# Performance work log

Hardware: AMD Instinct MI355X
Metric: run time of the kernel (lower is better)

Reference implementation:

```python
import jax, jax.numpy as jnp
import numpy as np

D, H, KVH, HD = 2048, 16, 8, 128
D1, D2 = 32, 64  # get_decompose_dim(2048)
BITS = 8


def fake_quant(x, bits=BITS):
    # per-row (last-axis) symmetric fake quant with straight-through estimator
    qmax = float(2 ** (bits - 1) - 1)
    s = jnp.maximum(jnp.max(jnp.abs(x), axis=-1, keepdims=True) / qmax, 1e-8)
    q = jnp.clip(jnp.round(x / s), -qmax, qmax) * s
    return x + jax.lax.stop_gradient(q - x)


def rotate_half(x):
    h = x.shape[-1] // 2
    return jnp.concatenate([-x[..., h:], x[..., :h]], axis=-1)


def setup_inputs() -> dict:
    key = jax.random.key(0)
    ks = jax.random.split(key, 10)
    B, S = 1, 2048
    hidden_states = jax.random.normal(ks[0], (B, S, D), jnp.float32)
    # rotary embeddings
    inv_freq = 1.0 / (10000.0 ** (jnp.arange(0, HD, 2, dtype=jnp.float32) / HD))
    t = jnp.arange(S, dtype=jnp.float32)
    freqs = t[:, None] * inv_freq[None, :]
    emb = jnp.concatenate([freqs, freqs], axis=-1)
    cos, sin = jnp.cos(emb)[None], jnp.sin(emb)[None]  # [1,S,HD]
    # projection weights
    Wq = jax.random.normal(ks[1], (H * HD, D), jnp.float32) * 0.02
    Wk = jax.random.normal(ks[2], (KVH * HD, D), jnp.float32) * 0.02
    Wv = jax.random.normal(ks[3], (KVH * HD, D), jnp.float32) * 0.02
    Wo = jax.random.normal(ks[4], (D, H * HD), jnp.float32) * 0.02
    # learned invertible transforms (near-identity for conditioning)
    L = jnp.eye(D1) + 0.02 * jax.random.normal(ks[5], (D1, D1), jnp.float32)
    R = jnp.eye(D2) + 0.02 * jax.random.normal(ks[6], (D2, D2), jnp.float32)
    diag = 1.0 + 0.1 * jax.random.uniform(ks[7], (D,), jnp.float32)
    Tk = jnp.eye(HD) + 0.02 * jax.random.normal(ks[8], (HD, HD), jnp.float32)
    Tv = jnp.eye(HD) + 0.02 * jax.random.normal(ks[9], (HD, HD), jnp.float32)
    return dict(hidden_states=hidden_states, cos=cos, sin=sin, Wq=Wq, Wk=Wk,
                Wv=Wv, Wo=Wo, L=L, R=R, diag=diag, Tk=Tk, Tv=Tv)


def reference(hidden_states, cos, sin, Wq, Wk, Wv, Wo, L, R, diag, Tk, Tv):
    B, S, _ = hidden_states.shape
    groups = H // KVH
    scale = HD ** -0.5
    # ---- ln_trans: x' = (x * diag) @ kron(L, R) ----
    P = diag[:, None] * jnp.kron(L, R)               # [D, D]
    Pinv = jnp.kron(jnp.linalg.inv(L), jnp.linalg.inv(R)) * (1.0 / diag)[None, :]
    x = hidden_states @ P
    x_q = fake_quant(x)                               # per-token activation quant
    # ---- QKV with transform fused into weights (qa_trans), then weight quant ----
    q = x_q @ fake_quant(Wq @ Pinv.T).T               # [B,S,H*HD]
    k = x_q @ fake_quant(Wk @ Pinv.T).T               # [B,S,KVH*HD]
    Wv_eff = jnp.einsum('hd,khD->kdD', Tv, (Wv @ Pinv.T).reshape(KVH, HD, D))
    v = x_q @ fake_quant(Wv_eff.reshape(KVH * HD, D)).T  # v already in Tv space
    # ---- heads + RoPE ----
    q = q.reshape(B, S, H, HD).transpose(0, 2, 1, 3)
    k = k.reshape(B, S, KVH, HD).transpose(0, 2, 1, 3)
    v = v.reshape(B, S, KVH, HD).transpose(0, 2, 1, 3)
    c, s_ = cos[:, None], sin[:, None]                # [1,1,S,HD]
    q = q * c + rotate_half(q) * s_
    k = k * c + rotate_half(k) * s_
    # ---- kcache trans + quant: q @ inv(Tk)^T, k @ Tk (dot product preserved) ----
    q = q @ jnp.linalg.inv(Tk).T
    k = fake_quant(k @ Tk)
    v = fake_quant(v)
    # ---- eager causal attention with GQA ----
    k = jnp.repeat(k, groups, axis=1)
    v = jnp.repeat(v, groups, axis=1)
    scores = jnp.einsum('bhqd,bhkd->bhqk', q, k) * scale
    mask = jnp.tril(jnp.ones((S, S), bool))
    scores = jnp.where(mask, scores, jnp.finfo(scores.dtype).min)
    w = jax.nn.softmax(scores, axis=-1)
    o = jnp.einsum('bhqk,bhkd->bhqd', w, v)
    o = o.transpose(0, 2, 1, 3).reshape(B, S, H * HD)
    # ---- undo vcache trans per head, then quantized o_proj ----
    o = (o.reshape(B, S, H, HD) @ jnp.linalg.inv(Tv)).reshape(B, S, H * HD)
    out = fake_quant(o) @ fake_quant(Wo).T
    return out
```

## Files before the change

### kernel.cpp

```cpp
#include <hip/hip_runtime.h>
#include <math.h>

typedef unsigned short u16;
typedef __attribute__((ext_vector_type(8))) short bf16x8;
typedef __attribute__((ext_vector_type(4))) float f32x4;

__device__ __forceinline__ u16 f2bf(float x) {
    union { float f; unsigned int u; } c; c.f = x;
    unsigned int r = c.u + 0x7fffu + ((c.u >> 16) & 1u);
    return (u16)(r >> 16);
}
__device__ __forceinline__ float bf2f(u16 h) {
    union { unsigned int u; float f; } c; c.u = ((unsigned int)h) << 16;
    return c.f;
}
__device__ __forceinline__ bf16x8 ld16(const u16* p) {
    bf16x8 r;
    ((uint2*)&r)[0] = *(const uint2*)p;
    ((uint2*)&r)[1] = *(const uint2*)(p + 4);
    return r;
}
__device__ __forceinline__ void st8(u16* dst, uint4 r) {
    *(uint2*)dst = make_uint2(r.x, r.y);
    *(uint2*)(dst + 4) = make_uint2(r.z, r.w);
}
__device__ __forceinline__ void cvt8(const float4& v0, const float4& v1,
                                     uint4& hi, uint4& lo) {
    float vv[8] = {v0.x, v0.y, v0.z, v0.w, v1.x, v1.y, v1.z, v1.w};
    u16 h[8], l[8];
#pragma unroll
    for (int e = 0; e < 8; ++e) {
        h[e] = f2bf(vv[e]);
        l[e] = f2bf(vv[e] - bf2f(h[e]));
    }
    hi.x = h[0] | ((unsigned)h[1] << 16); hi.y = h[2] | ((unsigned)h[3] << 16);
    hi.z = h[4] | ((unsigned)h[5] << 16); hi.w = h[6] | ((unsigned)h[7] << 16);
    lo.x = l[0] | ((unsigned)l[1] << 16); lo.y = l[2] | ((unsigned)l[3] << 16);
    lo.z = l[4] | ((unsigned)l[5] << 16); lo.w = l[6] | ((unsigned)l[7] << 16);
}

__global__ __launch_bounds__(1024) void p0_kernel(
    const float* __restrict__ A0, float* __restrict__ I0,
    const float* __restrict__ A1, float* __restrict__ I1,
    const float* __restrict__ A2, float* __restrict__ I2,
    const float* __restrict__ A3, float* __restrict__ I3,
    const float* __restrict__ X, const float* __restrict__ dg,
    const float* __restrict__ Lk, const float* __restrict__ Rk,
    u16* __restrict__ Yq, float* __restrict__ Ysc) {
    const int tid = threadIdx.x;
    if (blockIdx.x < 4) {
        __shared__ float rowbuf[2][128];
        const float* A; float* out; int N;
        switch (blockIdx.x) {
            case 0:  A = A0; out = I0; N = 32;  break;
            case 1:  A = A1; out = I1; N = 64;  break;
            case 2:  A = A2; out = I2; N = 128; break;
            default: A = A3; out = I3; N = 128; break;
        }
        const int i = tid >> 3, g = tid & 7, c0 = g * 16;
        const int rl = (i & 7) << 3;
        float r[16];
#pragma unroll
        for (int e = 0; e < 16; ++e) {
            int j = c0 + e;
            r[e] = (i < N && j < N) ? A[i * N + j] : ((i == j) ? 1.0f : 0.0f);
        }
        if (i == 0) {
            float ip = 1.0f / __shfl(r[0], rl, 64);
#pragma unroll
            for (int e = 0; e < 16; ++e)
                rowbuf[0][c0 + e] = (c0 + e == 0) ? ip : r[e] * ip;
        }
        __syncthreads();
        const int ng = N >> 4;
        for (int k16 = 0; k16 < ng; ++k16) {
#pragma unroll
            for (int e = 0; e < 16; ++e) {
                const int k = (k16 << 4) + e;
                const int pb = k & 1;
                float ci = __shfl(r[e], rl + k16, 64);
                float4 rb0 = *(const float4*)&rowbuf[pb][c0];
                float4 rb1 = *(const float4*)&rowbuf[pb][c0 + 4];
                float4 rb2 = *(const float4*)&rowbuf[pb][c0 + 8];
                float4 rb3 = *(const float4*)&rowbuf[pb][c0 + 12];
                float rb[16] = {rb0.x, rb0.y, rb0.z, rb0.w, rb1.x, rb1.y, rb1.z, rb1.w,
                                rb2.x, rb2.y, rb2.z, rb2.w, rb3.x, rb3.y, rb3.z, rb3.w};
                if (i == k) {
#pragma unroll
                    for (int e2 = 0; e2 < 16; ++e2) r[e2] = rb[e2];
                } else {
#pragma unroll
                    for (int e2 = 0; e2 < 16; ++e2) {
                        float v = (c0 + e2 == k) ? 0.0f : r[e2];
                        r[e2] = fmaf(-ci, rb[e2], v);
                    }
                }
                if (k + 1 < N && i == k + 1) {
                    const int en = (e + 1) & 15;
                    const int gn = (e == 15) ? k16 + 1 : k16;
                    float ip = 1.0f / __shfl(r[en], rl + gn, 64);
#pragma unroll
                    for (int e2 = 0; e2 < 16; ++e2)
                        rowbuf[pb ^ 1][c0 + e2] = (c0 + e2 == k + 1) ? ip : r[e2] * ip;
                }
                __syncthreads();
            }
        }
        if (i < N)
#pragma unroll
            for (int e = 0; e < 16; ++e) {
                int j = c0 + e;
                if (j < N) out[i * N + j] = r[e];
            }
    } else {
        __shared__ float Al[32 * 33];
        __shared__ float Bl[64 * 65];
        __shared__ float Tl[4][32 * 65];
        __shared__ float red[1024];
        {
            int c = tid >> 5, a = tid & 31;
            Al[c * 33 + a] = Lk[c * 32 + a];
        }
        for (int idx = tid; idx < 4096; idx += 1024) {
            int d = idx >> 6, b = idx & 63;
            Bl[d * 65 + b] = Rk[d * 64 + b];
        }
        __syncthreads();

        const int g = tid >> 8, t = tid & 255;
        const int row = (blockIdx.x - 4) * 4 + g;
        const int c = t >> 3, b0 = (t & 7) * 8;

        const float* xp = X + (size_t)row * 2048 + c * 64;
        const float* dgp = dg + c * 64;
        float tacc[8];
#pragma unroll
        for (int jj = 0; jj < 8; ++jj) tacc[jj] = 0.0f;
        for (int d0 = 0; d0 < 64; d0 += 4) {
            float4 xv4 = *(const float4*)(xp + d0);
            float4 dg4 = *(const float4*)(dgp + d0);
            float xs4[4] = {xv4.x * dg4.x, xv4.y * dg4.y, xv4.z * dg4.z, xv4.w * dg4.w};
#pragma unroll
            for (int e = 0; e < 4; ++e) {
                float xv = xs4[e];
#pragma unroll
                for (int jj = 0; jj < 8; ++jj)
                    tacc[jj] = fmaf(xv, Bl[(d0 + e) * 65 + b0 + jj], tacc[jj]);
            }
        }
#pragma unroll
        for (int jj = 0; jj < 8; ++jj) Tl[g][c * 65 + b0 + jj] = tacc[jj];
        __syncthreads();

        const int a = t >> 3;
        float y[8];
#pragma unroll
        for (int jj = 0; jj < 8; ++jj) y[jj] = 0.0f;
        for (int c2 = 0; c2 < 32; ++c2) {
            float av = Al[c2 * 33 + a];
#pragma unroll
            for (int jj = 0; jj < 8; ++jj)
                y[jj] = fmaf(av, Tl[g][c2 * 65 + b0 + jj], y[jj]);
        }

        float am = 0.0f;
#pragma unroll
        for (int jj = 0; jj < 8; ++jj) am = fmaxf(am, fabsf(y[jj]));
        red[tid] = am;
        __syncthreads();
        for (int s = 128; s > 0; s >>= 1) {
            if (t < s) red[tid] = fmaxf(red[tid], red[tid + s]);
            __syncthreads();
        }
        float scale = fmaxf(red[g << 8] / 127.0f, 1e-8f);
        if (t == 0) Ysc[row] = scale;
        u16 qq[8];
#pragma unroll
        for (int e = 0; e < 8; ++e) {
            float v = rintf(y[e] / scale);
            v = fminf(fmaxf(v, -127.0f), 127.0f);
            qq[e] = f2bf(v);
        }
        uint4 pk;
        pk.x = qq[0] | ((unsigned)qq[1] << 16); pk.y = qq[2] | ((unsigned)qq[3] << 16);
        pk.z = qq[4] | ((unsigned)qq[5] << 16); pk.w = qq[6] | ((unsigned)qq[7] << 16);
        *(uint4*)(Yq + (size_t)row * 2048 + t * 8) = pk;
    }
}

template <int TA, int TB, int OUTQ, int DIV>
__global__ __launch_bounds__(256) void kron_kernel(
    const float* __restrict__ X, const float* __restrict__ scIn,
    const float* __restrict__ A, const float* __restrict__ B,
    u16* __restrict__ Yq, float* __restrict__ Ysc, float* __restrict__ Yf) {
    __shared__ float Al[32 * 33];
    __shared__ float Bl[64 * 65];
    __shared__ float Xl[32 * 65];
    __shared__ float Tl[32 * 65];
    __shared__ float red[256];
    const int tid = threadIdx.x;
    for (int idx = tid; idx < 1024; idx += 256) {
        int c = idx >> 5, a = idx & 31;
        Al[c * 33 + a] = TA ? A[a * 32 + c] : A[c * 32 + a];
    }
    for (int idx = tid; idx < 4096; idx += 256) {
        int d = idx >> 6, b = idx & 63;
        Bl[d * 65 + b] = TB ? B[b * 64 + d] : B[d * 64 + b];
    }
    const int row = blockIdx.x;
    const float* xp = X + (size_t)row * 2048;
    for (int j = tid; j < 2048; j += 256) {
        float sc = DIV ? (1.0f / scIn[j]) : scIn[j];
        Xl[(j >> 6) * 65 + (j & 63)] = xp[j] * sc;
    }
    __syncthreads();

    const int c = tid >> 3, b0 = (tid & 7) * 8;
    float t[8];
#pragma unroll
    for (int jj = 0; jj < 8; ++jj) t[jj] = 0.0f;
    for (int d = 0; d < 64; ++d) {
        float xv = Xl[c * 65 + d];
#pragma unroll
        for (int jj = 0; jj < 8; ++jj)
            t[jj] = fmaf(xv, Bl[d * 65 + b0 + jj], t[jj]);
    }
#pragma unroll
    for (int jj = 0; jj < 8; ++jj) Tl[c * 65 + b0 + jj] = t[jj];
    __syncthreads();

    const int a = tid >> 3;
    float y[8];
#pragma unroll
    for (int jj = 0; jj < 8; ++jj) y[jj] = 0.0f;
    for (int c2 = 0; c2 < 32; ++c2) {
        float av = Al[c2 * 33 + a];
#pragma unroll
        for (int jj = 0; jj < 8; ++jj)
            y[jj] = fmaf(av, Tl[c2 * 65 + b0 + jj], y[jj]);
    }

    if (OUTQ) {
        float am = 0.0f;
#pragma unroll
        for (int jj = 0; jj < 8; ++jj) am = fmaxf(am, fabsf(y[jj]));
        red[tid] = am;
        __syncthreads();
        for (int s = 128; s > 0; s >>= 1) {
            if (tid < s) red[tid] = fmaxf(red[tid], red[tid + s]);
            __syncthreads();
        }
        float scale = fmaxf(red[0] / 127.0f, 1e-8f);
        if (tid == 0) Ysc[row] = scale;
        u16 qq[8];
#pragma unroll
        for (int e = 0; e < 8; ++e) {
            float v = rintf(y[e] / scale);
            v = fminf(fmaxf(v, -127.0f), 127.0f);
            qq[e] = f2bf(v);
        }
        uint4 pk;
        pk.x = qq[0] | ((unsigned)qq[1] << 16); pk.y = qq[2] | ((unsigned)qq[3] << 16);
        pk.z = qq[4] | ((unsigned)qq[5] << 16); pk.w = qq[6] | ((unsigned)qq[7] << 16);
        *(uint4*)(Yq + (size_t)row * 2048 + tid * 8) = pk;
    } else {
        float* yp = Yf + (size_t)row * 2048 + tid * 8;
        *(float4*)yp = make_float4(y[0], y[1], y[2], y[3]);
        *(float4*)(yp + 4) = make_float4(y[4], y[5], y[6], y[7]);
    }
}

__global__ void split_s_kernel(const float* __restrict__ in, int ld, int cols,
                               u16* __restrict__ hi, u16* __restrict__ lo) {
    int idx = (blockIdx.x * 256 + threadIdx.x) * 4;
    int r = idx / cols, c = idx % cols;
    float4 v = *(const float4*)(in + (size_t)r * ld + c);
    ushort4 h, l;
    h.x = f2bf(v.x); l.x = f2bf(v.x - bf2f(h.x));
    h.y = f2bf(v.y); l.y = f2bf(v.y - bf2f(h.y));
    h.z = f2bf(v.z); l.z = f2bf(v.z - bf2f(h.z));
    h.w = f2bf(v.w); l.w = f2bf(v.w - bf2f(h.w));
    *(ushort4*)(hi + idx) = h;
    *(ushort4*)(lo + idx) = l;
}

__global__ void split_t_kernel(const float* __restrict__ in, u16* __restrict__ hi,
                               u16* __restrict__ lo, int rows, int cols) {
    __shared__ float t[32][33];
    int bx = blockIdx.x, by = blockIdx.y;
    int lx = threadIdx.x & 31, ly = threadIdx.x >> 5;
    for (int r = ly; r < 32; r += 8)
        t[r][lx] = in[(size_t)(by * 32 + r) * cols + bx * 32 + lx];
    __syncthreads();
    for (int r = ly; r < 32; r += 8) {
        float v = t[lx][r];
        size_t o = (size_t)(bx * 32 + r) * rows + by * 32 + lx;
        u16 h = f2bf(v);
        hi[o] = h;
        lo[o] = f2bf(v - bf2f(h));
    }
}

__global__ void split_t3_kernel(const float* __restrict__ i0, u16* __restrict__ h0,
                                u16* __restrict__ l0,
                                const float* __restrict__ i1, u16* __restrict__ h1,
                                u16* __restrict__ l1,
                                const float* __restrict__ i2, u16* __restrict__ h2,
                                u16* __restrict__ l2) {
    __shared__ float t[32][33];
    const float* in; u16* hi; u16* lo;
    switch (blockIdx.z) {
        case 0:  in = i0; hi = h0; lo = l0; break;
        case 1:  in = i1; hi = h1; lo = l1; break;
        default: in = i2; hi = h2; lo = l2; break;
    }
    int bx = blockIdx.x, by = blockIdx.y;
    int lx = threadIdx.x & 31, ly = threadIdx.x >> 5;
    for (int r = ly; r < 32; r += 8)
        t[r][lx] = in[(size_t)(by * 32 + r) * 128 + bx * 32 + lx];
    __syncthreads();
    for (int r = ly; r < 32; r += 8) {
        float v = t[lx][r];
        size_t o = (size_t)(bx * 32 + r) * 128 + by * 32 + lx;
        u16 h = f2bf(v);
        hi[o] = h;
        lo[o] = f2bf(v - bf2f(h));
    }
}

__global__ __launch_bounds__(256) void gemm_kernel(
    const u16* __restrict__ Ah, const u16* __restrict__ Al, int lda, long aZ, int aDiv,
    const u16* __restrict__ Bh, const u16* __restrict__ Bl, int ldb, long bZ, int bDiv,
    float* __restrict__ C, int ldc, long cZ, int cDiv, int K, float alpha) {
    const int m0 = blockIdx.y * 128, n0 = blockIdx.x * 128;
    const int z = blockIdx.z;
    {
        long ao = (long)(z >> aDiv) * aZ;
        long bo = (long)(z >> bDiv) * bZ;
        Ah += ao; Al += ao; Bh += bo; Bl += bo;
    }
    __shared__ u16 Ash[2][2][128][36];
    __shared__ u16 Bsh[2][2][128][36];

    const int tid = threadIdx.x, lane = tid & 63, wave = tid >> 6;
    const int wr = wave >> 1, wc = wave & 1;
    const int fr = lane & 15, fg8 = (lane >> 4) * 8;
    const int srow = tid >> 2, cc8 = (tid & 3) * 8;

    f32x4 acc[4][4];
#pragma unroll
    for (int m = 0; m < 4; ++m)
#pragma unroll
        for (int n = 0; n < 4; ++n) acc[m][n] = (f32x4)0.0f;

    uint4 rah0, rah1, ral0, ral1, rbh0, rbh1, rbl0, rbl1;
    const size_t aoff0 = (size_t)(m0 + srow) * lda + cc8;
    const size_t aoff1 = aoff0 + (size_t)64 * lda;
    const size_t boff0 = (size_t)(n0 + srow) * ldb + cc8;
    const size_t boff1 = boff0 + (size_t)64 * ldb;

#define G_LOAD(k0) { \
    rah0 = *(const uint4*)(Ah + aoff0 + (k0)); rah1 = *(const uint4*)(Ah + aoff1 + (k0)); \
// ... 22 lines not shown
#pragma unroll
        for (int m = 0; m < 4; ++m) {
            bf16x8 ah = ld16(&Ash[cur][0][wr * 64 + m * 16 + fr][fg8]);
            bf16x8 al = ld16(&Ash[cur][1][wr * 64 + m * 16 + fr][fg8]);
#pragma unroll
            for (int n = 0; n < 4; ++n) {
                acc[m][n] = __builtin_amdgcn_mfma_f32_16x16x32_bf16(ah, bh[n], acc[m][n], 0, 0, 0);
                acc[m][n] = __builtin_amdgcn_mfma_f32_16x16x32_bf16(ah, bl[n], acc[m][n], 0, 0, 0);
                acc[m][n] = __builtin_amdgcn_mfma_f32_16x16x32_bf16(al, bh[n], acc[m][n], 0, 0, 0);
            }
        }
        if (ik + 1 < nk) G_STORE(cur ^ 1);
        __syncthreads();
        cur ^= 1;
    }
    const long co = (long)(z >> cDiv) * cZ;
#pragma unroll
    for (int m = 0; m < 4; ++m) {
        int row_b = m0 + wr * 64 + m * 16 + (fg8 >> 1);
#pragma unroll
        for (int n = 0; n < 4; ++n) {
            int col = n0 + wc * 64 + n * 16 + fr;
#pragma unroll
            for (int j = 0; j < 4; ++j)
                C[co + (long)(row_b + j) * ldc + col] = alpha * acc[m][n][j];
        }
    }
#undef G_LOAD
#undef G_STORE
}

__global__ __launch_bounds__(256) void gemm_qk_kernel(
    const float* __restrict__ QKVf,
    const u16* __restrict__ iTk_h, const u16* __restrict__ iTk_l,
    const u16* __restrict__ TkT_h, const u16* __restrict__ TkT_l,
    float* __restrict__ q2f, float* __restrict__ k2f) {
    const int m0 = blockIdx.y * 128;
    const int z = blockIdx.z;
    const bool isQ = (z < 16);
    const float* A = QKVf + (isQ ? z * 128 : 2048 + (z - 16) * 128);
    const u16* Bh = isQ ? iTk_h : TkT_h;
    const u16* Bl = isQ ? iTk_l : TkT_l;
    float* C = isQ ? (q2f + z * 128) : (k2f + (z - 16) * 128);
    const int ldc = isQ ? 2048 : 1024;
    const int lda = 4096, ldb = 128, K = 128;

    __shared__ u16 Ash[2][2][128][36];
    __shared__ u16 Bsh[2][2][128][36];
    const int tid = threadIdx.x, lane = tid & 63, wave = tid >> 6;
    const int wr = wave >> 1, wc = wave & 1;
    const int fr = lane & 15, fg8 = (lane >> 4) * 8;
    const int srow = tid >> 2, cc8 = (tid & 3) * 8;

    f32x4 acc[4][4];
#pragma unroll
    for (int m = 0; m < 4; ++m)
#pragma unroll
        for (int n = 0; n < 4; ++n) acc[m][n] = (f32x4)0.0f;

    float4 a00, a01, a10, a11;
    uint4 rbh0, rbh1, rbl0, rbl1;
    const size_t aoff0 = (size_t)(m0 + srow) * lda + cc8;
    const size_t aoff1 = aoff0 + (size_t)64 * lda;
    const size_t boff0 = (size_t)srow * ldb + cc8;
    const size_t boff1 = boff0 + (size_t)64 * ldb;

#define GQ_LOAD(k0) { \
    a00 = *(const float4*)(A + aoff0 + (k0)); a01 = *(const float4*)(A + aoff0 + (k0) + 4); \
    a10 = *(const float4*)(A + aoff1 + (k0)); a11 = *(const float4*)(A + aoff1 + (k0) + 4); \
    rbh0 = *(const uint4*)(Bh + boff0 + (k0)); rbh1 = *(const uint4*)(Bh + boff1 + (k0)); \
    rbl0 = *(const uint4*)(Bl + boff0 + (k0)); rbl1 = *(const uint4*)(Bl + boff1 + (k0)); }
#define GQ_STORE(b) { \
    uint4 h0_, l0_, h1_, l1_; \
    cvt8(a00, a01, h0_, l0_); cvt8(a10, a11, h1_, l1_); \
    st8(&Ash[b][0][srow][cc8], h0_); st8(&Ash[b][0][srow + 64][cc8], h1_); \
    st8(&Ash[b][1][srow][cc8], l0_); st8(&Ash[b][1][srow + 64][cc8], l1_); \
    st8(&Bsh[b][0][srow][cc8], rbh0); st8(&Bsh[b][0][srow + 64][cc8], rbh1); \
    st8(&Bsh[b][1][srow][cc8], rbl0); st8(&Bsh[b][1][srow + 64][cc8], rbl1); }

    const int nk = K >> 5;
    GQ_LOAD(0);
    GQ_STORE(0);
    __syncthreads();
    int cur = 0;
    for (int ik = 0; ik < nk; ++ik) {
        if (ik + 1 < nk) GQ_LOAD((ik + 1) << 5);
        bf16x8 bh[4], bl[4];
#pragma unroll
        for (int n = 0; n < 4; ++n) {
            bh[n] = ld16(&Bsh[cur][0][wc * 64 + n * 16 + fr][fg8]);
            bl[n] = ld16(&Bsh[cur][1][wc * 64 + n * 16 + fr][fg8]);
        }
#pragma unroll
        for (int m = 0; m < 4; ++m) {
            bf16x8 ah = ld16(&Ash[cur][0][wr * 64 + m * 16 + fr][fg8]);
            bf16x8 al = ld16(&Ash[cur][1][wr * 64 + m * 16 + fr][fg8]);
#pragma unroll
            for (int n = 0; n < 4; ++n) {
                acc[m][n] = __builtin_amdgcn_mfma_f32_16x16x32_bf16(ah, bh[n], acc[m][n], 0, 0, 0);
                acc[m][n] = __builtin_amdgcn_mfma_f32_16x16x32_bf16(ah, bl[n], acc[m][n], 0, 0, 0);
                acc[m][n] = __builtin_amdgcn_mfma_f32_16x16x32_bf16(al, bh[n], acc[m][n], 0, 0, 0);
            }
        }
        if (ik + 1 < nk) GQ_STORE(cur ^ 1);
        __syncthreads();
        cur ^= 1;
    }
#pragma unroll
    for (int m = 0; m < 4; ++m) {
        int row_b = m0 + wr * 64 + m * 16 + (fg8 >> 1);
#pragma unroll
        for (int n = 0; n < 4; ++n) {
            int col = wc * 64 + n * 16 + fr;
#pragma unroll
            for (int j = 0; j < 4; ++j)
                C[(long)(row_b + j) * ldc + col] = acc[m][n][j];
        }
    }
#undef GQ_LOAD
#undef GQ_STORE
}

__global__ __launch_bounds__(256) void gemm_o2_kernel(
    const float* __restrict__ o01, const float* __restrict__ ml,
    const u16* __restrict__ Bh, const u16* __restrict__ Bl,
    float* __restrict__ C) {
    const int m0 = blockIdx.y * 128;
    const int z = blockIdx.z;
    const int ldb = 128, K = 128, ldc = 2048;
    __shared__ u16 Ash[2][2][128][36];
    __shared__ u16 Bsh[2][2][128][36];
    const int tid = threadIdx.x, lane = tid & 63, wave = tid >> 6;
    const int wr = wave >> 1, wc = wave & 1;
    const int fr = lane & 15, fg8 = (lane >> 4) * 8;
    const int srow = tid >> 2, cc8 = (tid & 3) * 8;

    f32x4 acc[4][4];
#pragma unroll
    for (int m = 0; m < 4; ++m)
#pragma unroll
        for (int n = 0; n < 4; ++n) acc[m][n] = (f32x4)0.0f;

    const int rs0 = z * 2048 + m0 + srow;
    const int rs1 = rs0 + 64;
    float w0a, w1a, w0b, w1b;
    {
        float ma0 = ml[rs0], la0 = ml[32768 + rs0];
        float ma1 = ml[65536 + rs0], la1 = ml[98304 + rs0];
        float mm = fmaxf(ma0, ma1);
        float e0 = exp2f(ma0 - mm), e1 = exp2f(ma1 - mm);
        float linv = 1.0f / (la0 * e0 + la1 * e1);
        w0a = e0 * linv; w1a = e1 * linv;
        float mb0 = ml[rs1], lb0 = ml[32768 + rs1];
// ... 227 lines not shown
        vr[q] = *(const float4*)(p + q * 4);
        m = fmaxf(m, fmaxf(fmaxf(fabsf(vr[q].x), fabsf(vr[q].y)),
                           fmaxf(fabsf(vr[q].z), fabsf(vr[q].w))));
    }
    m = fmaxf(m, __shfl_xor(m, 1));
    m = fmaxf(m, __shfl_xor(m, 2));
    float scale = fmaxf(m / 127.0f, 1e-8f);
    if ((t & 3) == 0) vs[s * 8 + g] = scale;
#pragma unroll
    for (int q = 0; q < 8; ++q) {
        float vv[4] = {vr[q].x, vr[q].y, vr[q].z, vr[q].w};
#pragma unroll
        for (int e = 0; e < 4; ++e) {
            float qv = rintf(vv[e] / scale);
            qv = fminf(fmaxf(qv, -127.0f), 127.0f);
            tile[dc + q * 4 + e][sl] = f2bf(qv);
        }
    }
    __syncthreads();
    const int d = t >> 1, sc0 = (t & 1) * 32;
    u16* dst = vTi + (size_t)(g * 128 + d) * 2048 + st * 64 + sc0;
#pragma unroll
    for (int q = 0; q < 4; ++q) {
        u16 tmp[8];
#pragma unroll
        for (int e = 0; e < 8; ++e) tmp[e] = tile[d][sc0 + q * 8 + e];
        uint4 v;
        v.x = tmp[0] | ((unsigned)tmp[1] << 16); v.y = tmp[2] | ((unsigned)tmp[3] << 16);
        v.z = tmp[4] | ((unsigned)tmp[5] << 16); v.w = tmp[6] | ((unsigned)tmp[7] << 16);
        *(uint4*)(dst + q * 8) = v;
    }
}

__global__ void rope_kernel(float* __restrict__ x, int ld, int cb,
                            const float* __restrict__ c, const float* __restrict__ s,
                            int nh) {
    int idx = blockIdx.x * 256 + threadIdx.x;
    int d = idx & 63;
    int t = idx >> 6;
    int h = t % nh;
    int sq = t / nh;
    size_t base = (size_t)sq * ld + cb + h * 128;
    float a = x[base + d], b = x[base + d + 64];
    float c1 = c[sq * 128 + d], s1 = s[sq * 128 + d];
    float c2 = c[sq * 128 + d + 64], s2 = s[sq * 128 + d + 64];
    x[base + d] = a * c1 - b * s1;
    x[base + d + 64] = b * c2 + a * s2;
}

__global__ void add2_kernel(const float* __restrict__ a, const float* __restrict__ b,
                            float* __restrict__ o) {
    int i = (blockIdx.x * 256 + threadIdx.x) * 4;
    float4 x = *(const float4*)(a + i);
    float4 y = *(const float4*)(b + i);
    x.x += y.x; x.y += y.y; x.z += y.z; x.w += y.w;
    *(float4*)(o + i) = x;
}

__global__ __launch_bounds__(256, 2) void flash_kernel(
    const float* __restrict__ q2f,
    const u16* __restrict__ k2i, const float* __restrict__ ksc,
    const u16* __restrict__ vTi, const float* __restrict__ vsc,
    float* __restrict__ obuf, float* __restrict__ mlbuf) {
    const int h = blockIdx.x, part = blockIdx.y, qt = 31 - blockIdx.z, g = h >> 1;
    __shared__ u16 Ksh[2][64 * 128];
    __shared__ u16 Vsh[2][128 * 64];
    __shared__ u16 Psh[4][16 * 64];
    __shared__ float Kss[2][64];
    __shared__ float Vss[2][64];

    const int tid = threadIdx.x, lane = tid & 63, w = tid >> 6;
    const int lc = lane & 15, lg = lane >> 4;
    const float scale = 0.08838834764831845f;
    const float LOG2E = 1.4426950408889634f;
    const float THR = 10.0f;

    bf16x8 qh[4], ql[4];
    {
        int s = qt * 64 + w * 16 + lc;
        const float* qp = q2f + (size_t)s * 2048 + h * 128 + lg * 8;
#pragma unroll
        for (int kk = 0; kk < 4; ++kk) {
// ... 180 lines not shown
    const float* diag   = (const float*)d_in[9];
    const float* Tkp    = (const float*)d_in[10];
    const float* Tvp    = (const float*)d_in[11];
    float* out = (float*)d_out;

    const size_t MiB = 1ull << 20;
    char* W = (char*)d_ws;
    auto F = [&](size_t mb) { return (float*)(W + mb * MiB); };
    auto U = [&](size_t mb) { return (u16*)(W + mb * MiB); };
    const long HP2 = 2097152;

    float* dsc   = (float*)d_out;
    float* invL  = dsc;
    float* invR  = dsc + 1024;
    float* invTk = dsc + 5120;
    float* invTv = dsc + 21504;
    u16* sm = (u16*)(dsc + 37888);
    u16* invTk_sh = sm;              u16* invTk_sl = sm + 16384;
    u16* TkT_sh   = sm + 2 * 16384;  u16* TkT_sl   = sm + 3 * 16384;
    u16* invTvT_sh= sm + 4 * 16384;  u16* invTvT_sl= sm + 5 * 16384;
    u16* TvT_sh   = sm + 6 * 16384;  u16* TvT_sl   = sm + 7 * 16384;

    float* xs    = F(88);
    float* wqkvs = xs + 2048;
    float* wqs   = wqkvs;
    float* wks   = wqkvs + 2048;
    float* wvs   = wqkvs + 3072;
    float* k2s   = wqkvs + 4096;
    float* vs    = k2s + 16384;
    float* o2s   = vs + 16384;
    float* wos   = o2s + 2048;

    u16* Xi = U(0);
    p0_kernel<<<516, 1024, 0, stream>>>(Lp, invL, Rp, invR, Tkp, invTk, Tvp, invTv,
                                        hidden, diag, Lp, Rp, Xi, xs);
    split_s_kernel<<<16, 256, 0, stream>>>(invTk, 128, 128, invTk_sh, invTk_sl);
    split_t3_kernel<<<dim3(4, 4, 3), 256, 0, stream>>>(
        Tkp, TkT_sh, TkT_sl, invTv, invTvT_sh, invTvT_sl, Tvp, TvT_sh, TvT_sl);

    u16* WQKVi = U(8);
    u16* WVi   = U(20);
    float* WvP = F(24);
    kron_kernel<1, 1, 1, 1><<<2048, 256, 0, stream>>>(Wq, diag, invL, invR, WQKVi, wqs, 0);
    kron_kernel<1, 1, 1, 1><<<1024, 256, 0, stream>>>(Wk, diag, invL, invR, U(16), wks, 0);
    kron_kernel<1, 1, 0, 1><<<1024, 256, 0, stream>>>(Wv, diag, invL, invR, 0, 0, WvP);

    u16* WVPt_s = U(32);
    split_t_kernel<<<dim3(64, 32), 256, 0, stream>>>(WvP, WVPt_s, WVPt_s + HP2, 1024, 2048);
    float* WVf = F(72);
    gemm_kernel<<<dim3(16, 1, 8), 256, 0, stream>>>(
        TvT_sh, TvT_sl, 128, 0, 0, WVPt_s, WVPt_s + HP2, 1024, 128, 0,
        WVf, 2048, (long)128 * 2048, 0, 128, 1.0f);
    rowquant_int_kernel<<<1024, 256, 0, stream>>>(WVf, WVi, wvs, 2048);

    float* QKVf = F(40);
    gemm_int_kernel<<<dim3(32, 16), 256, 0, stream>>>(Xi, 2048, xs, WQKVi, 2048, wqkvs,
                                                      QKVf, 4096, 0, 0, 0, 2048);

    rope_kernel<<<8192, 256, 0, stream>>>(QKVf, 4096, 0, cosp, sinp, 16);
    rope_kernel<<<4096, 256, 0, stream>>>(QKVf, 4096, 2048, cosp, sinp, 8);

    float* q2f = F(72);
    float* k2f = F(32);
    gemm_qk_kernel<<<dim3(1, 16, 24), 256, 0, stream>>>(
        QKVf, invTk_sh, invTk_sl, TkT_sh, TkT_sl, q2f, k2f);
    u16* k2i = U(8);
    rowquant_w_kernel<<<4096, 256, 0, stream>>>(k2f, k2i, k2s);

    u16* vTi = U(16);
    quantT_v_kernel<<<dim3(32, 8), 256, 0, stream>>>(QKVf, vTi, vs);

    float* o01 = F(40);
    float* ml  = F(32);
    flash_kernel<<<dim3(16, 2, 32), 256, 0, stream>>>(q2f, k2i, k2s, vTi, vs, o01, ml);

    float* o2f = F(16);
    gemm_o2_kernel<<<dim3(1, 16, 16), 256, 0, stream>>>(
        o01, ml, invTvT_sh, invTvT_sl, o2f);
    u16* o2i = U(32);
    u16* Woi = U(40);
    rowquant2_kernel<<<4096, 256, 0, stream>>>(o2f, o2i, o2s, Wo, Woi, wos);
    float* C0 = F(48);
    gemm_int_kernel<<<dim3(16, 16, 2), 256, 0, stream>>>(o2i, 2048, o2s, Woi, 2048, wos,
                                                         C0, 2048, 1024, 1024, 4194304, 1024);
    add2_kernel<<<4096, 256, 0, stream>>>(C0, C0 + 4194304, out);

    (void)in_sizes; (void)n_in; (void)out_size; (void)ws_size;
}
```

Before: 451.2 us.

## Merge setup kernels into fewer launches and fuse RoPE into QK transform GEMM

Reorganises the preprocessing phase: matrix inversions, Kronecker transforms of activations and weights, and transpose-splits are packed into two large multi-role kernels plus a small split kernel, replacing several separate launches. The Wq/Wk/Wv Kronecker transforms now process four rows per 1024-thread block. RoPE is applied on the fly inside the gemm_qk loads instead of in two separate passes over QKV, removing a read-modify-write of the q/k activations. In exchange, the GEMM A-loads double and it also reads cos/sin, and the Tk/Tv inversions now run inside the wide weight-transform kernel, so their serial cost can stretch that launch.

```diff
diff --git a/kernel.cpp b/kernel.cpp
--- a/kernel.cpp
+++ b/kernel.cpp
@@ -39,130 +39,125 @@
     lo.z = l[4] | ((unsigned)l[5] << 16); lo.w = l[6] | ((unsigned)l[7] << 16);
 }
 
-__global__ __launch_bounds__(1024) void p0_kernel(
-    const float* __restrict__ A0, float* __restrict__ I0,
-    const float* __restrict__ A1, float* __restrict__ I1,
-    const float* __restrict__ A2, float* __restrict__ I2,
-    const float* __restrict__ A3, float* __restrict__ I3,
-    const float* __restrict__ X, const float* __restrict__ dg,
-    const float* __restrict__ Lk, const float* __restrict__ Rk,
-    u16* __restrict__ Yq, float* __restrict__ Ysc) {
-    const int tid = threadIdx.x;
-    if (blockIdx.x < 4) {
-        __shared__ float rowbuf[2][128];
-        const float* A; float* out; int N;
-        switch (blockIdx.x) {
-            case 0:  A = A0; out = I0; N = 32;  break;
-            case 1:  A = A1; out = I1; N = 64;  break;
-            case 2:  A = A2; out = I2; N = 128; break;
-            default: A = A3; out = I3; N = 128; break;
-        }
-        const int i = tid >> 3, g = tid & 7, c0 = g * 16;
-        const int rl = (i & 7) << 3;
-        float r[16];
+__device__ void gj_body(const float* __restrict__ A, float* __restrict__ out,
+                        int N, float (*rowbuf)[128], int tid) {
+    const int i = tid >> 3, g = tid & 7, c0 = g * 16;
+    const int rl = (i & 7) << 3;
+    float r[16];
+#pragma unroll
+    for (int e = 0; e < 16; ++e) {
+        int j = c0 + e;
+        r[e] = (i < N && j < N) ? A[i * N + j] : ((i == j) ? 1.0f : 0.0f);
+    }
+    if (i == 0) {
+        float ip = 1.0f / __shfl(r[0], rl, 64);
+#pragma unroll
+        for (int e = 0; e < 16; ++e)
+            rowbuf[0][c0 + e] = (c0 + e == 0) ? ip : r[e] * ip;
+    }
+    __syncthreads();
+    const int ng = N >> 4;
+    for (int k16 = 0; k16 < ng; ++k16) {
+#pragma unroll
+        for (int e = 0; e < 16; ++e) {
+            const int k = (k16 << 4) + e;
+            const int pb = k & 1;
+            float ci = __shfl(r[e], rl + k16, 64);
+            float4 rb0 = *(const float4*)&rowbuf[pb][c0];
+            float4 rb1 = *(const float4*)&rowbuf[pb][c0 + 4];
+            float4 rb2 = *(const float4*)&rowbuf[pb][c0 + 8];
+            float4 rb3 = *(const float4*)&rowbuf[pb][c0 + 12];
+            float rb[16] = {rb0.x, rb0.y, rb0.z, rb0.w, rb1.x, rb1.y, rb1.z, rb1.w,
+                            rb2.x, rb2.y, rb2.z, rb2.w, rb3.x, rb3.y, rb3.z, rb3.w};
+            if (i == k) {
+#pragma unroll
+                for (int e2 = 0; e2 < 16; ++e2) r[e2] = rb[e2];
+            } else {
+#pragma unroll
+                for (int e2 = 0; e2 < 16; ++e2) {
+                    float v = (c0 + e2 == k) ? 0.0f : r[e2];
+                    r[e2] = fmaf(-ci, rb[e2], v);
+                }
+            }
+            if (k + 1 < N && i == k + 1) {
+                const int en = (e + 1) & 15;
+                const int gn = (e == 15) ? k16 + 1 : k16;
+                float ip = 1.0f / __shfl(r[en], rl + gn, 64);
+#pragma unroll
+                for (int e2 = 0; e2 < 16; ++e2)
+                    rowbuf[pb ^ 1][c0 + e2] = (c0 + e2 == k + 1) ? ip : r[e2] * ip;
+            }
+            __syncthreads();
+        }
+    }
+    if (i < N)
 #pragma unroll
         for (int e = 0; e < 16; ++e) {
             int j = c0 + e;
-            r[e] = (i < N && j < N) ? A[i * N + j] : ((i == j) ? 1.0f : 0.0f);
-        }
-        if (i == 0) {
-            float ip = 1.0f / __shfl(r[0], rl, 64);
-#pragma unroll
-            for (int e = 0; e < 16; ++e)
-                rowbuf[0][c0 + e] = (c0 + e == 0) ? ip : r[e] * ip;
-        }
-        __syncthreads();
-        const int ng = N >> 4;
-        for (int k16 = 0; k16 < ng; ++k16) {
-#pragma unroll
-            for (int e = 0; e < 16; ++e) {
-                const int k = (k16 << 4) + e;
-                const int pb = k & 1;
-                float ci = __shfl(r[e], rl + k16, 64);
-                float4 rb0 = *(const float4*)&rowbuf[pb][c0];
-                float4 rb1 = *(const float4*)&rowbuf[pb][c0 + 4];
-                float4 rb2 = *(const float4*)&rowbuf[pb][c0 + 8];
-                float4 rb3 = *(const float4*)&rowbuf[pb][c0 + 12];
-                float rb[16] = {rb0.x, rb0.y, rb0.z, rb0.w, rb1.x, rb1.y, rb1.z, rb1.w,
-                                rb2.x, rb2.y, rb2.z, rb2.w, rb3.x, rb3.y, rb3.z, rb3.w};
-                if (i == k) {
-#pragma unroll
-                    for (int e2 = 0; e2 < 16; ++e2) r[e2] = rb[e2];
-                } else {
-#pragma unroll
-                    for (int e2 = 0; e2 < 16; ++e2) {
-                        float v = (c0 + e2 == k) ? 0.0f : r[e2];
-                        r[e2] = fmaf(-ci, rb[e2], v);
-                    }
-                }
-                if (k + 1 < N && i == k + 1) {
-                    const int en = (e + 1) & 15;
-                    const int gn = (e == 15) ? k16 + 1 : k16;
-                    float ip = 1.0f / __shfl(r[en], rl + gn, 64);
-#pragma unroll
-                    for (int e2 = 0; e2 < 16; ++e2)
-                        rowbuf[pb ^ 1][c0 + e2] = (c0 + e2 == k + 1) ? ip : r[e2] * ip;
-                }
-                __syncthreads();
-            }
-        }
-        if (i < N)
-#pragma unroll
-            for (int e = 0; e < 16; ++e) {
-                int j = c0 + e;
-                if (j < N) out[i * N + j] = r[e];
-            }
-    } else {
-        __shared__ float Al[32 * 33];
-        __shared__ float Bl[64 * 65];
-        __shared__ float Tl[4][32 * 65];
-        __shared__ float red[1024];
-        {
-            int c = tid >> 5, a = tid & 31;
-            Al[c * 33 + a] = Lk[c * 32 + a];
-        }
-        for (int idx = tid; idx < 4096; idx += 1024) {
-            int d = idx >> 6, b = idx & 63;
-            Bl[d * 65 + b] = Rk[d * 64 + b];
-        }
-        __syncthreads();
-
-        const int g = tid >> 8, t = tid & 255;
-        const int row = (blockIdx.x - 4) * 4 + g;
-        const int c = t >> 3, b0 = (t & 7) * 8;
-
-        const float* xp = X + (size_t)row * 2048 + c * 64;
-        const float* dgp = dg + c * 64;
-        float tacc[8];
-#pragma unroll
-        for (int jj = 0; jj < 8; ++jj) tacc[jj] = 0.0f;
-        for (int d0 = 0; d0 < 64; d0 += 4) {
-            float4 xv4 = *(const float4*)(xp + d0);
-            float4 dg4 = *(const float4*)(dgp + d0);
-            float xs4[4] = {xv4.x * dg4.x, xv4.y * dg4.y, xv4.z * dg4.z, xv4.w * dg4.w};
-#pragma unroll
-            for (int e = 0; e < 4; ++e) {
-                float xv = xs4[e];
-#pragma unroll
-                for (int jj = 0; jj < 8; ++jj)
-                    tacc[jj] = fmaf(xv, Bl[(d0 + e) * 65 + b0 + jj], tacc[jj]);
-            }
-        }
-#pragma unroll
-        for (int jj = 0; jj < 8; ++jj) Tl[g][c * 65 + b0 + jj] = tacc[jj];
-        __syncthreads();
-
-        const int a = t >> 3;
-        float y[8];
-#pragma unroll
-        for (int jj = 0; jj < 8; ++jj) y[jj] = 0.0f;
-        for (int c2 = 0; c2 < 32; ++c2) {
-            float av = Al[c2 * 33 + a];
+            if (j < N) out[i * N + j] = r[e];
+        }
+}
+
+template <int TA, int TB, int OUTQ, int DIV>
+__device__ void kron4_body(const float* __restrict__ X, const float* __restrict__ scIn,
+                           const float* __restrict__ A, const float* __restrict__ B,
+                           u16* __restrict__ Yq, float* __restrict__ Ysc,
+                           float* __restrict__ Yf, int row0, int tid,
+                           float* Al, float* Bl, float (*Tl)[32 * 65], float* red) {
+    {
+        int c = tid >> 5, a = tid & 31;
+        Al[c * 33 + a] = TA ? A[a * 32 + c] : A[c * 32 + a];
+    }
+    for (int idx = tid; idx < 4096; idx += 1024) {
+        int d = idx >> 6, b = idx & 63;
+        Bl[d * 65 + b] = TB ? B[b * 64 + d] : B[d * 64 + b];
+    }
+    __syncthreads();
+
+    const int g = tid >> 8, t = tid & 255;
+    const int row = row0 + g;
+    const int c = t >> 3, b0 = (t & 7) * 8;
+
+    const float* xp = X + (size_t)row * 2048 + c * 64;
+    const float* sp = scIn + c * 64;
+    float tacc[8];
+#pragma unroll
+    for (int jj = 0; jj < 8; ++jj) tacc[jj] = 0.0f;
+    for (int d0 = 0; d0 < 64; d0 += 4) {
+        float4 xv4 = *(const float4*)(xp + d0);
+        float4 sc4 = *(const float4*)(sp + d0);
+        float xs4[4];
+        if (DIV) {
+            xs4[0] = xv4.x * (1.0f / sc4.x); xs4[1] = xv4.y * (1.0f / sc4.y);
+            xs4[2] = xv4.z * (1.0f / sc4.z); xs4[3] = xv4.w * (1.0f / sc4.w);
+        } else {
+            xs4[0] = xv4.x * sc4.x; xs4[1] = xv4.y * sc4.y;
+            xs4[2] = xv4.z * sc4.z; xs4[3] = xv4.w * sc4.w;
+        }
+#pragma unroll
+        for (int e = 0; e < 4; ++e) {
+            float xv = xs4[e];
 #pragma unroll
             for (int jj = 0; jj < 8; ++jj)
-                y[jj] = fmaf(av, Tl[g][c2 * 65 + b0 + jj], y[jj]);
-        }
-
+                tacc[jj] = fmaf(xv, Bl[(d0 + e) * 65 + b0 + jj], tacc[jj]);
+        }
+    }
+#pragma unroll
+    for (int jj = 0; jj < 8; ++jj) Tl[g][c * 65 + b0 + jj] = tacc[jj];
+    __syncthreads();
+
+    const int a = t >> 3;
+    float y[8];
+#pragma unroll
+    for (int jj = 0; jj < 8; ++jj) y[jj] = 0.0f;
+    for (int c2 = 0; c2 < 32; ++c2) {
+        float av = Al[c2 * 33 + a];
+#pragma unroll
+        for (int jj = 0; jj < 8; ++jj)
+            y[jj] = fmaf(av, Tl[g][c2 * 65 + b0 + jj], y[jj]);
+    }
+
+    if (OUTQ) {
         float am = 0.0f;
 #pragma unroll
         for (int jj = 0; jj < 8; ++jj) am = fmaxf(am, fabsf(y[jj]));
@@ -185,103 +180,98 @@
         pk.x = qq[0] | ((unsigned)qq[1] << 16); pk.y = qq[2] | ((unsigned)qq[3] << 16);
         pk.z = qq[4] | ((unsigned)qq[5] << 16); pk.w = qq[6] | ((unsigned)qq[7] << 16);
         *(uint4*)(Yq + (size_t)row * 2048 + t * 8) = pk;
-    }
-}
-
-template <int TA, int TB, int OUTQ, int DIV>
-__global__ __launch_bounds__(256) void kron_kernel(
-    const float* __restrict__ X, const float* __restrict__ scIn,
-    const float* __restrict__ A, const float* __restrict__ B,
-    u16* __restrict__ Yq, float* __restrict__ Ysc, float* __restrict__ Yf) {
+    } else {
+        float* yp = Yf + (size_t)row * 2048 + t * 8;
+        *(float4*)yp = make_float4(y[0], y[1], y[2], y[3]);
+        *(float4*)(yp + 4) = make_float4(y[4], y[5], y[6], y[7]);
+    }
+}
+
+__device__ void tsplit_body(const float* __restrict__ in, u16* __restrict__ hi,
+                            u16* __restrict__ lo, int tid) {
+    for (int idx = tid; idx < 16384; idx += 1024) {
+        int r = idx >> 7, c = idx & 127;
+        float v = in[r * 128 + c];
+        u16 h = f2bf(v);
+        hi[c * 128 + r] = h;
+        lo[c * 128 + r] = f2bf(v - bf2f(h));
+    }
+}
+
+__global__ __launch_bounds__(1024) void p0a_kernel(
+    const float* __restrict__ Lp, float* __restrict__ invL,
+    const float* __restrict__ Rp, float* __restrict__ invR,
+    const float* __restrict__ hidden, const float* __restrict__ dg,
+    u16* __restrict__ Xi, float* __restrict__ xs,
+    const float* __restrict__ Tkp, u16* __restrict__ TkT_sh, u16* __restrict__ TkT_sl,
+    const float* __restrict__ Tvp, u16* __restrict__ TvT_sh, u16* __restrict__ TvT_sl) {
+    __shared__ float rowbuf[2][128];
     __shared__ float Al[32 * 33];
     __shared__ float Bl[64 * 65];
-    __shared__ float Xl[32 * 65];
-    __shared__ float Tl[32 * 65];
-    __shared__ float red[256];
+    __shared__ float Tl[4][32 * 65];
+    __shared__ float red[1024];
     const int tid = threadIdx.x;
-    for (int idx = tid; idx < 1024; idx += 256) {
-        int c = idx >> 5, a = idx & 31;
-        Al[c * 33 + a] = TA ? A[a * 32 + c] : A[c * 32 + a];
-    }
-    for (int idx = tid; idx < 4096; idx += 256) {
-        int d = idx >> 6, b = idx & 63;
-        Bl[d * 65 + b] = TB ? B[b * 64 + d] : B[d * 64 + b];
-    }
-    const int row = blockIdx.x;
-    const float* xp = X + (size_t)row * 2048;
-    for (int j = tid; j < 2048; j += 256) {
-        float sc = DIV ? (1.0f / scIn[j]) : scIn[j];
-        Xl[(j >> 6) * 65 + (j & 63)] = xp[j] * sc;
-    }
-    __syncthreads();
-
-    const int c = tid >> 3, b0 = (tid & 7) * 8;
-    float t[8];
-#pragma unroll
-    for (int jj = 0; jj < 8; ++jj) t[jj] = 0.0f;
-    for (int d = 0; d < 64; ++d) {
-        float xv = Xl[c * 65 + d];
-#pragma unroll
-        for (int jj = 0; jj < 8; ++jj)
-            t[jj] = fmaf(xv, Bl[d * 65 + b0 + jj], t[jj]);
-    }
-#pragma unroll
-    for (int jj = 0; jj < 8; ++jj) Tl[c * 65 + b0 + jj] = t[jj];
-    __syncthreads();
-
-    const int a = tid >> 3;
-    float y[8];
-#pragma unroll
-    for (int jj = 0; jj < 8; ++jj) y[jj] = 0.0f;
-    for (int c2 = 0; c2 < 32; ++c2) {
-        float av = Al[c2 * 33 + a];
-#pragma unroll
-        for (int jj = 0; jj < 8; ++jj)
-            y[jj] = fmaf(av, Tl[c2 * 65 + b0 + jj], y[jj]);
-    }
-
-    if (OUTQ) {
-        float am = 0.0f;
-#pragma unroll
-        for (int jj = 0; jj < 8; ++jj) am = fmaxf(am, fabsf(y[jj]));
-        red[tid] = am;
-        __syncthreads();
-        for (int s = 128; s > 0; s >>= 1) {
-            if (tid < s) red[tid] = fmaxf(red[tid], red[tid + s]);
-            __syncthreads();
-        }
-        float scale = fmaxf(red[0] / 127.0f, 1e-8f);
-        if (tid == 0) Ysc[row] = scale;
-        u16 qq[8];
-#pragma unroll
-        for (int e = 0; e < 8; ++e) {
-            float v = rintf(y[e] / scale);
-            v = fminf(fmaxf(v, -127.0f), 127.0f);
-            qq[e] = f2bf(v);
-        }
-        uint4 pk;
-        pk.x = qq[0] | ((unsigned)qq[1] << 16); pk.y = qq[2] | ((unsigned)qq[3] << 16);
-        pk.z = qq[4] | ((unsigned)qq[5] << 16); pk.w = qq[6] | ((unsigned)qq[7] << 16);
-        *(uint4*)(Yq + (size_t)row * 2048 + tid * 8) = pk;
+    const int b = blockIdx.x;
+    if (b == 0) {
+        gj_body(Lp, invL, 32, rowbuf, tid);
+    } else if (b == 1) {
+        gj_body(Rp, invR, 64, rowbuf, tid);
+    } else if (b < 514) {
+        kron4_body<0, 0, 1, 0>(hidden, dg, Lp, Rp, Xi, xs, 0, (b - 2) * 4, tid,
+                               Al, Bl, Tl, red);
+    } else if (b == 514) {
+        tsplit_body(Tkp, TkT_sh, TkT_sl, tid);
     } else {
-        float* yp = Yf + (size_t)row * 2048 + tid * 8;
-        *(float4*)yp = make_float4(y[0], y[1], y[2], y[3]);
-        *(float4*)(yp + 4) = make_float4(y[4], y[5], y[6], y[7]);
-    }
-}
-
-__global__ void split_s_kernel(const float* __restrict__ in, int ld, int cols,
-                               u16* __restrict__ hi, u16* __restrict__ lo) {
-    int idx = (blockIdx.x * 256 + threadIdx.x) * 4;
-    int r = idx / cols, c = idx % cols;
-    float4 v = *(const float4*)(in + (size_t)r * ld + c);
-    ushort4 h, l;
-    h.x = f2bf(v.x); l.x = f2bf(v.x - bf2f(h.x));
-    h.y = f2bf(v.y); l.y = f2bf(v.y - bf2f(h.y));
-    h.z = f2bf(v.z); l.z = f2bf(v.z - bf2f(h.z));
-    h.w = f2bf(v.w); l.w = f2bf(v.w - bf2f(h.w));
-    *(ushort4*)(hi + idx) = h;
-    *(ushort4*)(lo + idx) = l;
+        tsplit_body(Tvp, TvT_sh, TvT_sl, tid);
+    }
+}
+
+__global__ __launch_bounds__(1024) void p0b_kernel(
+    const float* __restrict__ Tkp, float* __restrict__ invTk,
+    const float* __restrict__ Tvp, float* __restrict__ invTv,
+    const float* __restrict__ Wq, const float* __restrict__ Wk,
+    const float* __restrict__ Wv, const float* __restrict__ dg,
+    const float* __restrict__ invL, const float* __restrict__ invR,
+    u16* __restrict__ WQi, float* __restrict__ wqs,
+    u16* __restrict__ WKi, float* __restrict__ wks,
+    float* __restrict__ WvP) {
+    __shared__ float rowbuf[2][128];
+    __shared__ float Al[32 * 33];
+    __shared__ float Bl[64 * 65];
+    __shared__ float Tl[4][32 * 65];
+    __shared__ float red[1024];
+    const int tid = threadIdx.x;
+    const int b = blockIdx.x;
+    if (b == 0) {
+        gj_body(Tkp, invTk, 128, rowbuf, tid);
+    } else if (b == 1) {
+        gj_body(Tvp, invTv, 128, rowbuf, tid);
+    } else if (b < 514) {
+        kron4_body<1, 1, 1, 1>(Wq, dg, invL, invR, WQi, wqs, 0, (b - 2) * 4, tid,
+                               Al, Bl, Tl, red);
+    } else if (b < 770) {
+        kron4_body<1, 1, 1, 1>(Wk, dg, invL, invR, WKi, wks, 0, (b - 514) * 4, tid,
+                               Al, Bl, Tl, red);
+    } else {
+        kron4_body<1, 1, 0, 1>(Wv, dg, invL, invR, 0, 0, WvP, (b - 770) * 4, tid,
+                               Al, Bl, Tl, red);
+    }
+}
+
+__global__ __launch_bounds__(1024) void ps_kernel(
+    const float* __restrict__ invTk, u16* __restrict__ ik_h, u16* __restrict__ ik_l,
+    const float* __restrict__ invTv, u16* __restrict__ ivT_h, u16* __restrict__ ivT_l) {
+    const int tid = threadIdx.x;
+    if (blockIdx.x == 0) {
+        for (int idx = tid; idx < 16384; idx += 1024) {
+            float v = invTk[idx];
+            u16 h = f2bf(v);
+            ik_h[idx] = h;
+            ik_l[idx] = f2bf(v - bf2f(h));
+        }
+    } else {
+        tsplit_body(invTv, ivT_h, ivT_l, tid);
+    }
 }
 
 __global__ void split_t_kernel(const float* __restrict__ in, u16* __restrict__ hi,
@@ -301,33 +291,6 @@
     }
 }
 
-__global__ void split_t3_kernel(const float* __restrict__ i0, u16* __restrict__ h0,
-                                u16* __restrict__ l0,
-                                const float* __restrict__ i1, u16* __restrict__ h1,
-                                u16* __restrict__ l1,
-                                const float* __restrict__ i2, u16* __restrict__ h2,
-                                u16* __restrict__ l2) {
-    __shared__ float t[32][33];
-    const float* in; u16* hi; u16* lo;
-    switch (blockIdx.z) {
-        case 0:  in = i0; hi = h0; lo = l0; break;
-        case 1:  in = i1; hi = h1; lo = l1; break;
-        default: in = i2; hi = h2; lo = l2; break;
-    }
-    int bx = blockIdx.x, by = blockIdx.y;
-    int lx = threadIdx.x & 31, ly = threadIdx.x >> 5;
-    for (int r = ly; r < 32; r += 8)
-        t[r][lx] = in[(size_t)(by * 32 + r) * 128 + bx * 32 + lx];
-    __syncthreads();
-    for (int r = ly; r < 32; r += 8) {
-        float v = t[lx][r];
-        size_t o = (size_t)(bx * 32 + r) * 128 + by * 32 + lx;
-        u16 h = f2bf(v);
-        hi[o] = h;
-        lo[o] = f2bf(v - bf2f(h));
-    }
-}
-
 __global__ __launch_bounds__(256) void gemm_kernel(
     const u16* __restrict__ Ah, const u16* __restrict__ Al, int lda, long aZ, int aDiv,
     const u16* __restrict__ Bh, const u16* __restrict__ Bl, int ldb, long bZ, int bDiv,
@@ -416,6 +379,7 @@
 
 __global__ __launch_bounds__(256) void gemm_qk_kernel(
     const float* __restrict__ QKVf,
+    const float* __restrict__ cosp, const float* __restrict__ sinp,
     const u16* __restrict__ iTk_h, const u16* __restrict__ iTk_l,
     const u16* __restrict__ TkT_h, const u16* __restrict__ TkT_l,
     float* __restrict__ q2f, float* __restrict__ k2f) {
@@ -448,10 +412,36 @@
     const size_t aoff1 = aoff0 + (size_t)64 * lda;
     const size_t boff0 = (size_t)srow * ldb + cc8;
     const size_t boff1 = boff0 + (size_t)64 * ldb;
-
+    const size_t coff0 = (size_t)(m0 + srow) * 128 + cc8;
+    const size_t coff1 = coff0 + (size_t)64 * 128;
+
+#define ROPE4(va, vb, vc4, vs4, sg) make_float4( \
+    (va).x * (vc4).x + (sg) * (vb).x * (vs4).x, \
+    (va).y * (vc4).y + (sg) * (vb).y * (vs4).y, \
+    (va).z * (vc4).z + (sg) * (vb).z * (vs4).z, \
+    (va).w * (vc4).w + (sg) * (vb).w * (vs4).w)
 #define GQ_LOAD(k0) { \
-    a00 = *(const float4*)(A + aoff0 + (k0)); a01 = *(const float4*)(A + aoff0 + (k0) + 4); \
-    a10 = *(const float4*)(A + aoff1 + (k0)); a11 = *(const float4*)(A + aoff1 + (k0) + 4); \
+    const int d0_ = (k0) + cc8; \
+    const int po_ = (d0_ < 64) ? 64 : -64; \
+    const float sg_ = (d0_ < 64) ? -1.0f : 1.0f; \
+    float4 ax0 = *(const float4*)(A + aoff0 + (k0)); \
+    float4 ax1 = *(const float4*)(A + aoff0 + (k0) + 4); \
+    float4 ay0 = *(const float4*)(A + aoff0 + (k0) + po_); \
+    float4 ay1 = *(const float4*)(A + aoff0 + (k0) + 4 + po_); \
+    float4 pc0 = *(const float4*)(cosp + coff0 + (k0)); \
+    float4 pc1 = *(const float4*)(cosp + coff0 + (k0) + 4); \
+    float4 ps0 = *(const float4*)(sinp + coff0 + (k0)); \
+    float4 ps1 = *(const float4*)(sinp + coff0 + (k0) + 4); \
+    a00 = ROPE4(ax0, ay0, pc0, ps0, sg_); a01 = ROPE4(ax1, ay1, pc1, ps1, sg_); \
+    float4 bx0 = *(const float4*)(A + aoff1 + (k0)); \
+    float4 bx1 = *(const float4*)(A + aoff1 + (k0) + 4); \
+    float4 by0 = *(const float4*)(A + aoff1 + (k0) + po_); \
+    float4 by1 = *(const float4*)(A + aoff1 + (k0) + 4 + po_); \
+    float4 qc0 = *(const float4*)(cosp + coff1 + (k0)); \
+    float4 qc1 = *(const float4*)(cosp + coff1 + (k0) + 4); \
+    float4 qs0 = *(const float4*)(sinp + coff1 + (k0)); \
+    float4 qs1 = *(const float4*)(sinp + coff1 + (k0) + 4); \
+    a10 = ROPE4(bx0, by0, qc0, qs0, sg_); a11 = ROPE4(bx1, by1, qc1, qs1, sg_); \
     rbh0 = *(const uint4*)(Bh + boff0 + (k0)); rbh1 = *(const uint4*)(Bh + boff1 + (k0)); \
     rbl0 = *(const uint4*)(Bl + boff0 + (k0)); rbl1 = *(const uint4*)(Bl + boff1 + (k0)); }
 #define GQ_STORE(b) { \
@@ -503,6 +493,7 @@
     }
 #undef GQ_LOAD
 #undef GQ_STORE
+#undef ROPE4
 }
 
 __global__ __launch_bounds__(256) void gemm_o2_kernel(
@@ -796,22 +787,6 @@
     }
 }
 
-__global__ void rope_kernel(float* __restrict__ x, int ld, int cb,
-                            const float* __restrict__ c, const float* __restrict__ s,
-                            int nh) {
-    int idx = blockIdx.x * 256 + threadIdx.x;
-    int d = idx & 63;
-    int t = idx >> 6;
-    int h = t % nh;
-    int sq = t / nh;
-    size_t base = (size_t)sq * ld + cb + h * 128;
-    float a = x[base + d], b = x[base + d + 64];
-    float c1 = c[sq * 128 + d], s1 = s[sq * 128 + d];
-    float c2 = c[sq * 128 + d + 64], s2 = s[sq * 128 + d + 64];
-    x[base + d] = a * c1 - b * s1;
-    x[base + d + 64] = b * c2 + a * s2;
-}
-
 __global__ void add2_kernel(const float* __restrict__ a, const float* __restrict__ b,
                             float* __restrict__ o) {
     int i = (blockIdx.x * 256 + threadIdx.x) * 4;
@@ -1058,18 +1033,17 @@
     float* wos   = o2s + 2048;
 
     u16* Xi = U(0);
-    p0_kernel<<<516, 1024, 0, stream>>>(Lp, invL, Rp, invR, Tkp, invTk, Tvp, invTv,
-                                        hidden, diag, Lp, Rp, Xi, xs);
-    split_s_kernel<<<16, 256, 0, stream>>>(invTk, 128, 128, invTk_sh, invTk_sl);
-    split_t3_kernel<<<dim3(4, 4, 3), 256, 0, stream>>>(
-        Tkp, TkT_sh, TkT_sl, invTv, invTvT_sh, invTvT_sl, Tvp, TvT_sh, TvT_sl);
+    p0a_kernel<<<516, 1024, 0, stream>>>(Lp, invL, Rp, invR, hidden, diag, Xi, xs,
+                                         Tkp, TkT_sh, TkT_sl, Tvp, TvT_sh, TvT_sl);
 
     u16* WQKVi = U(8);
     u16* WVi   = U(20);
     float* WvP = F(24);
-    kron_kernel<1, 1, 1, 1><<<2048, 256, 0, stream>>>(Wq, diag, invL, invR, WQKVi, wqs, 0);
-    kron_kernel<1, 1, 1, 1><<<1024, 256, 0, stream>>>(Wk, diag, invL, invR, U(16), wks, 0);
-    kron_kernel<1, 1, 0, 1><<<1024, 256, 0, stream>>>(Wv, diag, invL, invR, 0, 0, WvP);
+    p0b_kernel<<<1026, 1024, 0, stream>>>(Tkp, invTk, Tvp, invTv, Wq, Wk, Wv, diag,
+                                          invL, invR, WQKVi, wqs, U(16), wks, WvP);
+
+    ps_kernel<<<2, 1024, 0, stream>>>(invTk, invTk_sh, invTk_sl,
+                                      invTv, invTvT_sh, invTvT_sl);
 
     u16* WVPt_s = U(32);
     split_t_kernel<<<dim3(64, 32), 256, 0, stream>>>(WvP, WVPt_s, WVPt_s + HP2, 1024, 2048);
@@ -1083,13 +1057,10 @@
     gemm_int_kernel<<<dim3(32, 16), 256, 0, stream>>>(Xi, 2048, xs, WQKVi, 2048, wqkvs,
                                                       QKVf, 4096, 0, 0, 0, 2048);
 
-    rope_kernel<<<8192, 256, 0, stream>>>(QKVf, 4096, 0, cosp, sinp, 16);
-    rope_kernel<<<4096, 256, 0, stream>>>(QKVf, 4096, 2048, cosp, sinp, 8);
-
     float* q2f = F(72);
     float* k2f = F(32);
     gemm_qk_kernel<<<dim3(1, 16, 24), 256, 0, stream>>>(
-        QKVf, invTk_sh, invTk_sl, TkT_sh, TkT_sl, q2f, k2f);
+        QKVf, cosp, sinp, invTk_sh, invTk_sl, TkT_sh, TkT_sl, q2f, k2f);
     u16* k2i = U(8);
     rowquant_w_kernel<<<4096, 256, 0, stream>>>(k2f, k2i, k2s);
 
```

After: 481.2 us. 1.07x slower.
